# Kernel tuning notes

Measured on AMD Instinct MI355X. Metric: run time of the kernel, lower is better.

The kernel has to match this reference:

```python
import jax, jax.numpy as jnp
import numpy as np

BETA = 100.0
EXTS = [("r1", 515, 32, 16), ("r1_1", 512, 32, 16), ("r2", 512, 48, 12), ("r2_2", 576, 48, 12),
        ("r3", 576, 64, 12), ("r3_3", 768, 96, 8), ("r4", 768, 128, 6), ("r4_4", 768, 160, 6),
        ("r5", 960, 192, 5), ("r5_5", 960, 224, 4)]


def _wn(v, g):
    # torch weight_norm(dim=0): w[o] = g[o] * v[o] / ||v[o]||  (norm over input dims)
    n = jnp.sqrt(jnp.sum(v * v, axis=-1, keepdims=True))
    return g[..., None] * v / n


def _softplus_b(z):
    # torch Softplus(beta): (1/beta) * log(1 + exp(beta*z))
    return jax.nn.softplus(BETA * z) / BETA


def _resnext(x, grad, v, g, b):
    # x: [B,Cin,N], grad: [B,N,Cin,3]; v: [L,c,Cin] -- L parallel 1x1-conv branches,
    # outputs concatenated along channels (each branch reads the SAME input x).
    w = _wn(v, g)                                             # [L,c,Cin]
    pre = jnp.einsum('lci,bin->blcn', w, x) + b[None, :, :, None]
    sg = jax.nn.sigmoid(BETA * pre)                           # softplus' = sigmoid(beta*pre)
    B, L, c, N = pre.shape
    x_out = _softplus_b(pre).reshape(B, L * c, N)
    g_out = jnp.einsum('lci,bnid->bnlcd', w, grad)            # analytic chain-rule matmul
    g_out = (sg.transpose(0, 3, 1, 2)[..., None] * g_out).reshape(B, N, L * c, 3)
    return x_out, g_out


def setup_inputs() -> dict:
    key = jax.random.key(0)
    ks = iter(jax.random.split(key, 64))
    B, N = 1, 4096
    d = {}
    d["input"] = jax.random.normal(next(ks), (B, N, 3), jnp.float32)
    d["latent"] = jax.random.normal(next(ks), (B, 256), jnp.float32) * 0.1
    d["c1_v"] = jax.random.normal(next(ks), (515, 259), jnp.float32) * np.float32(np.sqrt(2.0 / 259.0))
    d["c1_g"] = 1.0 + 0.01 * jax.random.normal(next(ks), (515,), jnp.float32)
    d["c1_b"] = jnp.zeros((515,), jnp.float32)
    for name, cin, c, L in EXTS:
        d[name + "_v"] = jax.random.normal(next(ks), (L, c, cin), jnp.float32) * np.float32(np.sqrt(2.0 / cin))
        d[name + "_g"] = 1.0 + 0.01 * jax.random.normal(next(ks), (L, c), jnp.float32)
        d[name + "_b"] = jnp.zeros((L, c), jnp.float32)
    d["c10_v"] = jax.random.normal(next(ks), (1, 896), jnp.float32) * 1e-4 + np.float32(np.sqrt(np.pi / 896.0))
    d["c10_g"] = 1.0 + 0.01 * jax.random.normal(next(ks), (1,), jnp.float32)
    d["c10_b"] = -jnp.ones((1,), jnp.float32)
    return d


def reference(input, latent, c1_v, c1_g, c1_b,
              r1_v, r1_g, r1_b, r1_1_v, r1_1_g, r1_1_b,
              r2_v, r2_g, r2_b, r2_2_v, r2_2_g, r2_2_b,
              r3_v, r3_g, r3_b, r3_3_v, r3_3_g, r3_3_b,
              r4_v, r4_g, r4_b, r4_4_v, r4_4_g, r4_4_b,
              r5_v, r5_g, r5_b, r5_5_v, r5_5_g, r5_5_b,
              c10_v, c10_g, c10_b):
    # ImplicitMap_fExtrator.forward with compute_grad=True, cat_latent=True
    B, N = input.shape[0], input.shape[1]
    lat = jnp.broadcast_to(latent[:, None, :], (B, N, latent.shape[-1]))
    input_con = jnp.concatenate([input, lat], axis=-1)        # [B,N,259]
    x = input_con.transpose(0, 2, 1)                           # [B,259,N]

    # first conv: is_first=True -> input grad = w[:, :3] (d/d xyz)
    w1 = _wn(c1_v, c1_g)                                       # [515,259]
    pre = jnp.einsum('ci,bin->bcn', w1, x) + c1_b[None, :, None]
    grad = jnp.broadcast_to(w1[:, :3][None, None, :, :], (B, N, 515, 3))
    grad = jax.nn.sigmoid(BETA * pre).transpose(0, 2, 1)[..., None] * grad
    x = _softplus_b(pre)

    ext_params = [(r1_v, r1_g, r1_b), (r1_1_v, r1_1_g, r1_1_b),
                  (r2_v, r2_g, r2_b), (r2_2_v, r2_2_g, r2_2_b),
                  (r3_v, r3_g, r3_b), (r3_3_v, r3_3_g, r3_3_b),
                  (r4_v, r4_g, r4_b), (r4_4_v, r4_4_g, r4_4_b),
                  (r5_v, r5_g, r5_b), (r5_5_v, r5_5_g, r5_5_b)]
    for v, g, b in ext_params:
        x, grad = _resnext(x, grad, v, g, b)

    w10 = _wn(c10_v, c10_g)                                    # [1,896]
    out = jnp.einsum('ci,bin->bcn', w10, x) + c10_b[None, :, None]  # [B,1,N]
    out_grad = jnp.einsum('ci,bnid->bncd', w10, grad)               # [B,N,1,3]
    return out, out_grad, input_con
```

## Files before the change

### kernel.cpp

```cpp
#include <hip/hip_runtime.h>
#include <hip/hip_bf16.h>


#define NPTS 4096
#define XS 968

typedef unsigned short u16;
typedef unsigned int   u32;
typedef __attribute__((ext_vector_type(8))) __bf16 bf16x8;
typedef __attribute__((ext_vector_type(4))) float  f32x4;

__device__ __forceinline__ float bf2f(u16 h) {
  return __uint_as_float(((u32)h) << 16);
}
__device__ __forceinline__ u16 f2bf(float f) {
  u32 u = __float_as_uint(f);
  u += 0x7fff + ((u >> 16) & 1);
  return (u16)(u >> 16);
}

__device__ __forceinline__ void act_sp_sg(float pre, float& sp, float& sg) {
  float z = 100.f * pre;
  float e = __expf(-fabsf(z));
  float r = 1.f / (1.f + e);
  float l = __logf(1.f + e) * 0.01f;
  if (z >= 0.f) { sg = r;       sp = pre + l; }
  else          { sg = 1.f - r; sp = l; }
}

__global__ __launch_bounds__(256)
void build_x0(const float* __restrict__ inp, const float* __restrict__ lat,
              u16* __restrict__ x0, float* __restrict__ con) {
  const int n = blockIdx.x;
  for (int i = threadIdx.x; i < 320; i += 256) {
    float v = (i < 3) ? inp[n * 3 + i] : ((i < 259) ? lat[i - 3] : 0.f);
    x0[(size_t)n * 320 + i] = f2bf(v);
    if (i < 259) con[(size_t)n * 259 + i] = v;
  }
}

struct WLayer { const float* v; const float* g; int Cin, Cout, KS, MF; size_t woff; };
struct WAll { WLayer L[11]; };

__global__ __launch_bounds__(256)
void wnormF(WAll wa, u16* __restrict__ Wf) {
  const WLayer L = wa.L[blockIdx.y];
  const int cb = blockIdx.x;
  if (cb >= L.MF) return;
  __shared__ float red[16][17];
  __shared__ float scl[16];
  const int t = threadIdx.x;
  {
    const int col16 = t & 15, kt = t >> 4;
    const int col = cb * 16 + col16;
    float ss = 0.f;
    if (col < L.Cout)
      for (int k = kt; k < L.Cin; k += 16) {
        float x = L.v[(size_t)col * L.Cin + k]; ss += x * x;
      }
    red[col16][kt] = ss;
  }
  __syncthreads();
  if (t < 16) {
    float s = 0.f;
#pragma unroll
    for (int j = 0; j < 16; ++j) s += red[t][j];
    const int c = cb * 16 + t;
    scl[t] = (c < L.Cout) ? L.g[c] / sqrtf(s) : 0.f;
  }
  __syncthreads();
  u32* dst = (u32*)(Wf + L.woff);
  const int lane = t >> 2, q = t & 3;
  const int vcol = cb * 16 + (lane & 15);
  const float sc = scl[lane & 15];
  const float* vrow = L.v + (size_t)vcol * L.Cin;
  const bool cok = vcol < L.Cout;
  for (int ks = 0; ks < L.KS; ++ks) {
    const int k0 = ks * 32 + (lane >> 4) * 8 + q * 2;
    u16 lo = 0, hi16 = 0;
    if (cok) {
      if (k0 < L.Cin)     lo   = f2bf(vrow[k0] * sc);
      if (k0 + 1 < L.Cin) hi16 = f2bf(vrow[k0 + 1] * sc);
    }
    dst[(size_t)(ks * L.MF + cb) * 128 + t] = (u32)lo | ((u32)hi16 << 16);
  }
}

struct FusedArgs {
  size_t woff[11];
  const float* bias[11];
  const float* v10; const float* g10; const float* b10;
};

template<int KS, int MF, int COUT>
__device__ __forceinline__ void layer_mid(const u16* __restrict__ Wf,
                                          const float* __restrict__ bias,
                                          u16* __restrict__ X,
                                          int w, int lane, int lcol, int hi) {
  constexpr int NF = (MF + 11) / 12;
  f32x4 acc[4][NF];
#pragma unroll
  for (int s = 0; s < 4; ++s)
#pragma unroll
    for (int i = 0; i < NF; ++i) acc[s][i] = (f32x4){0.f, 0.f, 0.f, 0.f};

  const u16* wp = Wf + lane * 8;
  const int abase = lcol * XS + hi * 8;
  bf16x8 bA[NF], bB[NF];
#pragma unroll
  for (int i = 0; i < NF; ++i)
    if (w + 12 * i < MF)
      bA[i] = *(const bf16x8*)(wp + (size_t)(w + 12 * i) * 512);

#pragma unroll 1
  for (int ks = 0; ks < KS; ks += 2) {
    bf16x8 af[4];
#pragma unroll
    for (int s = 0; s < 4; ++s)
      af[s] = *(const bf16x8*)(X + abase + s * 16 * XS + ks * 32);
#pragma unroll
    for (int i = 0; i < NF; ++i)
      if (w + 12 * i < MF)
        bB[i] = *(const bf16x8*)(wp + (size_t)((ks + 1) * MF + w + 12 * i) * 512);
#pragma unroll
    for (int i = 0; i < NF; ++i)
      if (w + 12 * i < MF)
#pragma unroll
        for (int s = 0; s < 4; ++s)
          acc[s][i] = __builtin_amdgcn_mfma_f32_16x16x32_bf16(af[s], bA[i], acc[s][i], 0, 0, 0);
#pragma unroll
    for (int s = 0; s < 4; ++s)
      af[s] = *(const bf16x8*)(X + abase + s * 16 * XS + ks * 32 + 32);
    if (ks + 2 < KS) {
#pragma unroll
      for (int i = 0; i < NF; ++i)
        if (w + 12 * i < MF)
          bA[i] = *(const bf16x8*)(wp + (size_t)((ks + 2) * MF + w + 12 * i) * 512);
    }
#pragma unroll
    for (int i = 0; i < NF; ++i)
      if (w + 12 * i < MF)
#pragma unroll
        for (int s = 0; s < 4; ++s)
          acc[s][i] = __builtin_amdgcn_mfma_f32_16x16x32_bf16(af[s], bB[i], acc[s][i], 0, 0, 0);
  }
  __syncthreads();
#pragma unroll
  for (int i = 0; i < NF; ++i) {
    const int cb = w + 12 * i;
    if (cb < MF) {
      const int col = cb * 16 + lcol;
      const bool ok = col < COUT;
      const float bc = ok ? bias[col] : 0.f;
#pragma unroll
      for (int r = 0; r < 4; ++r) {
        const int p = hi * 4 + r;
        float sp = 0.f, sg = 0.f;
        if (ok) act_sp_sg(acc[0][i][r] + bc, sp, sg);
        X[(0 * 16 + p) * XS + col] = f2bf(sp);
        X[(1 * 16 + p) * XS + col] = f2bf(ok ? sg * acc[1][i][r] : 0.f);
        X[(2 * 16 + p) * XS + col] = f2bf(ok ? sg * acc[2][i][r] : 0.f);
        X[(3 * 16 + p) * XS + col] = f2bf(ok ? sg * acc[3][i][r] : 0.f);
      }
    }
  }
  __syncthreads();
}

template<int KS, int MF, int COUT>
__device__ __forceinline__ void layer_first(const u16* __restrict__ Wf,
                                            const float* __restrict__ bias,
                                            u16* __restrict__ X,
                                            int w, int lane, int lcol, int hi) {
  constexpr int NF = (MF + 11) / 12;
  f32x4 acc[NF];
#pragma unroll
  for (int i = 0; i < NF; ++i) acc[i] = (f32x4){0.f, 0.f, 0.f, 0.f};
  const u16* wp = Wf + lane * 8;
  const int abase = lcol * XS + hi * 8;
  bf16x8 bA[NF], bB[NF];
#pragma unroll
  for (int i = 0; i < NF; ++i)
    if (w + 12 * i < MF)
      bA[i] = *(const bf16x8*)(wp + (size_t)(w + 12 * i) * 512);
#pragma unroll 1
  for (int ks = 0; ks < KS; ks += 2) {
    bf16x8 af0 = *(const bf16x8*)(X + abase + ks * 32);
#pragma unroll
    for (int i = 0; i < NF; ++i)
      if (w + 12 * i < MF)
        bB[i] = *(const bf16x8*)(wp + (size_t)((ks + 1) * MF + w + 12 * i) * 512);
#pragma unroll
    for (int i = 0; i < NF; ++i)
      if (w + 12 * i < MF)
        acc[i] = __builtin_amdgcn_mfma_f32_16x16x32_bf16(af0, bA[i], acc[i], 0, 0, 0);
    bf16x8 af1 = *(const bf16x8*)(X + abase + ks * 32 + 32);
    if (ks + 2 < KS) {
#pragma unroll
      for (int i = 0; i < NF; ++i)
        if (w + 12 * i < MF)
          bA[i] = *(const bf16x8*)(wp + (size_t)((ks + 2) * MF + w + 12 * i) * 512);
    }
#pragma unroll
    for (int i = 0; i < NF; ++i)
      if (w + 12 * i < MF)
        acc[i] = __builtin_amdgcn_mfma_f32_16x16x32_bf16(af1, bB[i], acc[i], 0, 0, 0);
  }
  __syncthreads();
#pragma unroll
  for (int i = 0; i < NF; ++i) {
    const int cb = w + 12 * i;
    if (cb < MF) {
      const int col = cb * 16 + lcol;
      const bool ok = col < COUT;
      float bc = 0.f, w0 = 0.f, w1 = 0.f, w2 = 0.f;
      if (ok) {
        bc = bias[col];
        const u16* wk = Wf + ((size_t)cb * 64 + lcol) * 8;
        w0 = bf2f(wk[0]); w1 = bf2f(wk[1]); w2 = bf2f(wk[2]);
      }
#pragma unroll
      for (int r = 0; r < 4; ++r) {
        const int p = hi * 4 + r;
        float sp = 0.f, sg = 0.f;
        if (ok) act_sp_sg(acc[i][r] + bc, sp, sg);
        X[(0 * 16 + p) * XS + col] = f2bf(sp);
        X[(1 * 16 + p) * XS + col] = f2bf(sg * w0);
        X[(2 * 16 + p) * XS + col] = f2bf(sg * w1);
        X[(3 * 16 + p) * XS + col] = f2bf(sg * w2);
      }
    }
  }
  __syncthreads();
}

__global__ __launch_bounds__(768, 1)
void fused_net(FusedArgs fa, const u16* __restrict__ WfAll,
               const u16* __restrict__ x0,
               float* __restrict__ out, float* __restrict__ outg) {
  __shared__ __align__(16) u16 X[64 * XS];
  __shared__ float fred[12];
  const int t = threadIdx.x;
  const int w = t >> 6, lane = t & 63;
  const int lcol = lane & 15, hi = lane >> 4;
  const int n0 = blockIdx.x * 16;

  for (int c = t; c < 640; c += 768) {
    const int row = c / 40, ch = c % 40;
    uint4 q = *reinterpret_cast<const uint4*>(x0 + (size_t)(n0 + row) * 320 + ch * 8);
    *reinterpret_cast<uint4*>(X + row * XS + ch * 8) = q;
  }
  __syncthreads();

  layer_first<10, 36, 515>(WfAll + fa.woff[0],  fa.bias[0],  X, w, lane, lcol, hi);
  layer_mid<18, 32, 512>(WfAll + fa.woff[1],  fa.bias[1],  X, w, lane, lcol, hi);
  layer_mid<16, 32, 512>(WfAll + fa.woff[2],  fa.bias[2],  X, w, lane, lcol, hi);
  layer_mid<16, 36, 576>(WfAll + fa.woff[3],  fa.bias[3],  X, w, lane, lcol, hi);
  layer_mid<18, 36, 576>(WfAll + fa.woff[4],  fa.bias[4],  X, w, lane, lcol, hi);
  layer_mid<18, 48, 768>(WfAll + fa.woff[5],  fa.bias[5],  X, w, lane, lcol, hi);
  layer_mid<24, 48, 768>(WfAll + fa.woff[6],  fa.bias[6],  X, w, lane, lcol, hi);
  layer_mid<24, 48, 768>(WfAll + fa.woff[7],  fa.bias[7],  X, w, lane, lcol, hi);
  layer_mid<24, 60, 960>(WfAll + fa.woff[8],  fa.bias[8],  X, w, lane, lcol, hi);
  layer_mid<30, 60, 960>(WfAll + fa.woff[9],  fa.bias[9],  X, w, lane, lcol, hi);
  layer_mid<30, 56, 896>(WfAll + fa.woff[10], fa.bias[10], X, w, lane, lcol, hi);

  float ss = 0.f;
  for (int k = t; k < 896; k += 768) { float x = fa.v10[k]; ss += x * x; }
#pragma unroll
  for (int off = 32; off > 0; off >>= 1) ss += __shfl_xor(ss, off);
  if (lane == 0) fred[w] = ss;
  __syncthreads();
  float tot = 0.f;
#pragma unroll
  for (int j = 0; j < 12; ++j) tot += fred[j];
  const float scale = fa.g10[0] / sqrtf(tot);

  for (int id = w; id < 64; id += 12) {
    const int s = id >> 4, p = id & 15;
    const u16* xr = X + (s * 16 + p) * XS;
    float d = 0.f;
#pragma unroll
    for (int j = 0; j < 14; ++j) {
      const int k = lane * 14 + j;
      d += fa.v10[k] * bf2f(xr[k]);
    }
    d *= scale;
#pragma unroll
    for (int off = 32; off > 0; off >>= 1) d += __shfl_xor(d, off);
    if (lane == 0) {
      if (s == 0) out[n0 + p] = d + fa.b10[0];
      else        outg[(size_t)(n0 + p) * 3 + (s - 1)] = d;
    }
  }
}

extern "C" void kernel_launch(void* const* d_in, const int* in_sizes, int n_in,
                              void* d_out, int out_size, void* d_ws, size_t ws_size,
                              hipStream_t stream) {
  static const int CIN [11] = {259,515,512,512,576,576,768,768,768,960,960};
  static const int COUT[11] = {515,512,512,576,576,768,768,768,960,960,896};
  static const int KS  [11] = {10,18,16,16,18,18,24,24,24,30,30};
  static const int MF  [11] = {36,32,32,36,36,48,48,48,60,60,56};

  size_t woff[12]; woff[0] = 0;
  for (int l = 0; l < 11; ++l)
    woff[l + 1] = woff[l] + (size_t)KS[l] * MF[l] * 512;

  char* ws = (char*)d_ws;
  u16* Wf = (u16*)ws;
  size_t off = (woff[11] * 2 + 255) & ~(size_t)255;
  u16* x0 = (u16*)(ws + off);

  float* out_sdf  = (float*)d_out;
  float* out_grad = out_sdf + NPTS;
  float* out_con  = out_sdf + NPTS + NPTS*3;

  build_x0<<<dim3(NPTS), dim3(256), 0, stream>>>(
      (const float*)d_in[0], (const float*)d_in[1], x0, out_con);

  WAll wa;
  for (int l = 0; l < 11; ++l) {
    wa.L[l].v = (const float*)d_in[2 + 3 * l];
    wa.L[l].g = (const float*)d_in[3 + 3 * l];
    wa.L[l].Cin = CIN[l]; wa.L[l].Cout = COUT[l];
    wa.L[l].KS = KS[l]; wa.L[l].MF = MF[l];
    wa.L[l].woff = woff[l];
  }
  wnormF<<<dim3(60, 11), dim3(256), 0, stream>>>(wa, Wf);

  FusedArgs fa;
  for (int l = 0; l < 11; ++l) {
    fa.woff[l] = woff[l];
    fa.bias[l] = (const float*)d_in[4 + 3 * l];
  }
  fa.v10 = (const float*)d_in[35];
  fa.g10 = (const float*)d_in[36];
  fa.b10 = (const float*)d_in[37];

  fused_net<<<dim3(NPTS / 16), dim3(768), 0, stream>>>(
      fa, Wf, x0, out_sdf, out_grad);
}
```

Before: 225.9 us.

## Fold input construction into fused kernel and fully unroll K loop with ring-buffered weights

Removes the separate build_x0 launch and its global round trip: the fused kernel now builds the bf16 input tile in shared memory directly from input and latent, and writes input_con itself. The K loops in both layer helpers are fully unrolled. Weight fragments sit in a two-slot register ring that is prefetched two steps ahead, replacing the hand-paired A/B steps. This saves one kernel launch and the x0 traffic, but full unrolling increases code size and may raise register pressure at 768 threads per block.

```diff
diff --git a/kernel.cpp b/kernel.cpp
--- a/kernel.cpp
+++ b/kernel.cpp
@@ -26,17 +26,6 @@
   float l = __logf(1.f + e) * 0.01f;
   if (z >= 0.f) { sg = r;       sp = pre + l; }
   else          { sg = 1.f - r; sp = l; }
-}
-
-__global__ __launch_bounds__(256)
-void build_x0(const float* __restrict__ inp, const float* __restrict__ lat,
-              u16* __restrict__ x0, float* __restrict__ con) {
-  const int n = blockIdx.x;
-  for (int i = threadIdx.x; i < 320; i += 256) {
-    float v = (i < 3) ? inp[n * 3 + i] : ((i < 259) ? lat[i - 3] : 0.f);
-    x0[(size_t)n * 320 + i] = f2bf(v);
-    if (i < 259) con[(size_t)n * 259 + i] = v;
-  }
 }
 
 struct WLayer { const float* v; const float* g; int Cin, Cout, KS, MF; size_t woff; };
@@ -105,44 +94,35 @@
     for (int i = 0; i < NF; ++i) acc[s][i] = (f32x4){0.f, 0.f, 0.f, 0.f};
 
   const u16* wp = Wf + lane * 8;
-  const int abase = lcol * XS + hi * 8;
-  bf16x8 bA[NF], bB[NF];
+  const u16* xa = X + lcol * XS + hi * 8;
+  bf16x8 bw[2][NF];
 #pragma unroll
   for (int i = 0; i < NF; ++i)
-    if (w + 12 * i < MF)
-      bA[i] = *(const bf16x8*)(wp + (size_t)(w + 12 * i) * 512);
-
-#pragma unroll 1
-  for (int ks = 0; ks < KS; ks += 2) {
+    if (w + 12 * i < MF) {
+      bw[0][i] = *(const bf16x8*)(wp + (size_t)(w + 12 * i) * 512);
+      bw[1][i] = *(const bf16x8*)(wp + (size_t)(MF + w + 12 * i) * 512);
+    }
+
+#pragma unroll
+  for (int ks = 0; ks < KS; ++ks) {
     bf16x8 af[4];
 #pragma unroll
     for (int s = 0; s < 4; ++s)
-      af[s] = *(const bf16x8*)(X + abase + s * 16 * XS + ks * 32);
-#pragma unroll
-    for (int i = 0; i < NF; ++i)
-      if (w + 12 * i < MF)
-        bB[i] = *(const bf16x8*)(wp + (size_t)((ks + 1) * MF + w + 12 * i) * 512);
-#pragma unroll
-    for (int i = 0; i < NF; ++i)
-      if (w + 12 * i < MF)
-#pragma unroll
-        for (int s = 0; s < 4; ++s)
-          acc[s][i] = __builtin_amdgcn_mfma_f32_16x16x32_bf16(af[s], bA[i], acc[s][i], 0, 0, 0);
-#pragma unroll
-    for (int s = 0; s < 4; ++s)
-      af[s] = *(const bf16x8*)(X + abase + s * 16 * XS + ks * 32 + 32);
+      af[s] = *(const bf16x8*)(xa + s * 16 * XS + ks * 32);
     if (ks + 2 < KS) {
 #pragma unroll
       for (int i = 0; i < NF; ++i)
         if (w + 12 * i < MF)
-          bA[i] = *(const bf16x8*)(wp + (size_t)((ks + 2) * MF + w + 12 * i) * 512);
+          bw[ks & 1][i] = *(const bf16x8*)(wp + (size_t)((ks + 2) * MF + w + 12 * i) * 512);
     }
 #pragma unroll
     for (int i = 0; i < NF; ++i)
-      if (w + 12 * i < MF)
+      if (w + 12 * i < MF) {
 #pragma unroll
         for (int s = 0; s < 4; ++s)
-          acc[s][i] = __builtin_amdgcn_mfma_f32_16x16x32_bf16(af[s], bB[i], acc[s][i], 0, 0, 0);
+          acc[s][i] = __builtin_amdgcn_mfma_f32_16x16x32_bf16(
+              af[s], bw[ks & 1][i], acc[s][i], 0, 0, 0);
+      }
   }
   __syncthreads();
 #pragma unroll
@@ -177,34 +157,27 @@
 #pragma unroll
   for (int i = 0; i < NF; ++i) acc[i] = (f32x4){0.f, 0.f, 0.f, 0.f};
   const u16* wp = Wf + lane * 8;
-  const int abase = lcol * XS + hi * 8;
-  bf16x8 bA[NF], bB[NF];
+  const u16* xa = X + lcol * XS + hi * 8;
+  bf16x8 bw[2][NF];
 #pragma unroll
   for (int i = 0; i < NF; ++i)
-    if (w + 12 * i < MF)
-      bA[i] = *(const bf16x8*)(wp + (size_t)(w + 12 * i) * 512);
-#pragma unroll 1
-  for (int ks = 0; ks < KS; ks += 2) {
-    bf16x8 af0 = *(const bf16x8*)(X + abase + ks * 32);
+    if (w + 12 * i < MF) {
+      bw[0][i] = *(const bf16x8*)(wp + (size_t)(w + 12 * i) * 512);
+      bw[1][i] = *(const bf16x8*)(wp + (size_t)(MF + w + 12 * i) * 512);
+    }
+#pragma unroll
+  for (int ks = 0; ks < KS; ++ks) {
+    bf16x8 af = *(const bf16x8*)(xa + ks * 32);
+    if (ks + 2 < KS) {
+#pragma unroll
+      for (int i = 0; i < NF; ++i)
+        if (w + 12 * i < MF)
+          bw[ks & 1][i] = *(const bf16x8*)(wp + (size_t)((ks + 2) * MF + w + 12 * i) * 512);
+    }
 #pragma unroll
     for (int i = 0; i < NF; ++i)
       if (w + 12 * i < MF)
-        bB[i] = *(const bf16x8*)(wp + (size_t)((ks + 1) * MF + w + 12 * i) * 512);
-#pragma unroll
-    for (int i = 0; i < NF; ++i)
-      if (w + 12 * i < MF)
-        acc[i] = __builtin_amdgcn_mfma_f32_16x16x32_bf16(af0, bA[i], acc[i], 0, 0, 0);
-    bf16x8 af1 = *(const bf16x8*)(X + abase + ks * 32 + 32);
-    if (ks + 2 < KS) {
-#pragma unroll
-      for (int i = 0; i < NF; ++i)
-        if (w + 12 * i < MF)
-          bA[i] = *(const bf16x8*)(wp + (size_t)((ks + 2) * MF + w + 12 * i) * 512);
-    }
-#pragma unroll
-    for (int i = 0; i < NF; ++i)
-      if (w + 12 * i < MF)
-        acc[i] = __builtin_amdgcn_mfma_f32_16x16x32_bf16(af1, bB[i], acc[i], 0, 0, 0);
+        acc[i] = __builtin_amdgcn_mfma_f32_16x16x32_bf16(af, bw[ks & 1][i], acc[i], 0, 0, 0);
   }
   __syncthreads();
 #pragma unroll
@@ -236,8 +209,9 @@
 
 __global__ __launch_bounds__(768, 1)
 void fused_net(FusedArgs fa, const u16* __restrict__ WfAll,
-               const u16* __restrict__ x0,
-               float* __restrict__ out, float* __restrict__ outg) {
+               const float* __restrict__ inp, const float* __restrict__ lat,
+               float* __restrict__ out, float* __restrict__ outg,
+               float* __restrict__ con) {
   __shared__ __align__(16) u16 X[64 * XS];
   __shared__ float fred[12];
   const int t = threadIdx.x;
@@ -245,10 +219,12 @@
   const int lcol = lane & 15, hi = lane >> 4;
   const int n0 = blockIdx.x * 16;
 
-  for (int c = t; c < 640; c += 768) {
-    const int row = c / 40, ch = c % 40;
-    uint4 q = *reinterpret_cast<const uint4*>(x0 + (size_t)(n0 + row) * 320 + ch * 8);
-    *reinterpret_cast<uint4*>(X + row * XS + ch * 8) = q;
+  for (int c = t; c < 16 * 320; c += 768) {
+    const int row = c / 320, i = c - row * 320;
+    const float v = (i < 3) ? inp[(size_t)(n0 + row) * 3 + i]
+                  : ((i < 259) ? lat[i - 3] : 0.f);
+    X[row * XS + i] = f2bf(v);
+    if (i < 259) con[(size_t)(n0 + row) * 259 + i] = v;
   }
   __syncthreads();
 
@@ -306,17 +282,11 @@
   for (int l = 0; l < 11; ++l)
     woff[l + 1] = woff[l] + (size_t)KS[l] * MF[l] * 512;
 
-  char* ws = (char*)d_ws;
-  u16* Wf = (u16*)ws;
-  size_t off = (woff[11] * 2 + 255) & ~(size_t)255;
-  u16* x0 = (u16*)(ws + off);
+  u16* Wf = (u16*)d_ws;
 
   float* out_sdf  = (float*)d_out;
   float* out_grad = out_sdf + NPTS;
   float* out_con  = out_sdf + NPTS + NPTS*3;
-
-  build_x0<<<dim3(NPTS), dim3(256), 0, stream>>>(
-      (const float*)d_in[0], (const float*)d_in[1], x0, out_con);
 
   WAll wa;
   for (int l = 0; l < 11; ++l) {
@@ -338,5 +308,6 @@
   fa.b10 = (const float*)d_in[37];
 
   fused_net<<<dim3(NPTS / 16), dim3(768), 0, stream>>>(
-      fa, Wf, x0, out_sdf, out_grad);
-}
+      fa, Wf, (const float*)d_in[0], (const float*)d_in[1],
+      out_sdf, out_grad, out_con);
+}
```

After: 234.3 us. +3.7%, slower.
